# Optimization experiments

Hardware: AMD Instinct MI355X
Metric: run time of the kernel (lower is better)

## Reference

```python
import jax, jax.numpy as jnp
import numpy as np

B, L, S, D = 16, 32, 128, 256
WIN = 9
NEG = -1e10
EPS = 1e-6


def _band_mask(seq_len, win_size):
    half = win_size // 2
    i = jnp.arange(seq_len)
    m = jnp.abs(i[:, None] - i[None, :]) <= half
    return m[None, None, :, :]


def setup_inputs() -> dict:
    key = jax.random.key(0)
    ks = jax.random.split(key, 12)
    H_s = jax.random.normal(ks[0], (B, L, S, D), dtype=jnp.float32)
    seg_mask = jnp.ones((B, L, 1, S), dtype=bool)
    s = 0.02
    return {
        "H_s": H_s,
        "seg_mask": seg_mask,
        "Wq": jax.random.normal(ks[1], (D, D), jnp.float32) * s,
        "Wk": jax.random.normal(ks[2], (D, D), jnp.float32) * s,
        "Wv": jax.random.normal(ks[3], (D, D), jnp.float32) * s,
        "Wh_w": jax.random.normal(ks[4], (D, 1), jnp.float32) * s,
        "Wh_b": jnp.zeros((1,), jnp.float32),
        "Wg_w": jax.random.normal(ks[5], (D, 1), jnp.float32) * s,
        "Wl_w": jax.random.normal(ks[6], (D, 1), jnp.float32) * s,
        "ln_g": jnp.ones((D,), jnp.float32),
        "ln_b": jnp.zeros((D,), jnp.float32),
        "feat_simi": _band_mask(S, WIN),
    }


def reference(H_s, seg_mask, Wq, Wk, Wv, Wh_w, Wh_b, Wg_w, Wl_w, ln_g, ln_b, feat_simi):
    d = H_s.shape[-1]
    scaling = jnp.asarray(d, H_s.dtype) ** 0.5
    Q = H_s @ Wq
    K = H_s @ Wk
    V = H_s @ Wv
    # shared scores, computed once: (B, L, S, S)
    GP = jnp.einsum('blqd,blkd->blqk', Q / scaling, K)
    GP = jnp.where(seg_mask, GP, NEG)  # global path mask
    G_Att = jnp.einsum('blqk,blkd->blqd', jax.nn.softmax(GP, axis=-1), V)
    LP = jnp.where(feat_simi, GP, NEG)  # local window mask on top
    L_Att = jnp.einsum('blqk,blkd->blqd', jax.nn.softmax(LP, axis=-1), V)
    gate = jax.nn.sigmoid((H_s @ Wh_w + Wh_b) + G_Att @ Wg_w + L_Att @ Wl_w)
    Fusion = gate * L_Att + (1.0 - gate) * G_Att
    x = Fusion + H_s
    mu = jnp.mean(x, axis=-1, keepdims=True)
    var = jnp.var(x, axis=-1, keepdims=True)
    return ln_g * (x - mu) / jnp.sqrt(var + EPS) + ln_b
```

## Files before the change

kernel.cpp:

```cpp
#include <hip/hip_runtime.h>
#include <hip/hip_bf16.h>
#include <stdint.h>


#define NBL   512
#define SS    128
#define DD    256
#define BLKT  512
#define QSTR  264
#define VSTR  136
#define WSTR  40
#define NEGF  (-1e10f)

#define OFF_Q    0
#define OFF_KV   (SS * QSTR * 2)
#define KV_BYTES (DD * VSTR * 2)
#define OFF_W5   (OFF_KV + KV_BYTES)
#define SMEM_BYTES (OFF_W5 + 5 * DD * 4)
#define BUF_BYTES (DD * WSTR * 2)

typedef __attribute__((ext_vector_type(8))) short bf16x8;
typedef __attribute__((ext_vector_type(4))) float floatx4;

__device__ __forceinline__ uint32_t f2bf1(float f) {
  uint32_t u = __float_as_uint(f);
  return (u + 0x7fffu + ((u >> 16) & 1u)) >> 16;
}
__device__ __forceinline__ short f2bs(float f) { return (short)f2bf1(f); }
__device__ __forceinline__ uint32_t packbf(float a, float b) {
  return f2bf1(a) | (f2bf1(b) << 16);
}
__device__ __forceinline__ float qredSum(float v) {
  v += __shfl_xor(v, 1, 64); v += __shfl_xor(v, 2, 64);
  v += __shfl_xor(v, 4, 64); v += __shfl_xor(v, 8, 64);
  return v;
}
__device__ __forceinline__ float qredMax(float v) {
  v = fmaxf(v, __shfl_xor(v, 1, 64)); v = fmaxf(v, __shfl_xor(v, 2, 64));
  v = fmaxf(v, __shfl_xor(v, 4, 64)); v = fmaxf(v, __shfl_xor(v, 8, 64));
  return v;
}

#define LBAR() asm volatile("s_waitcnt lgkmcnt(0)\n\ts_barrier" ::: "memory")

#define LD_SLICE(DST, KS)                                          \
  {                                                                \
    _Pragma("unroll")                                              \
    for (int i = 0; i < 4; ++i) {                                  \
      const int ge = (KS) * 32 + (eb0 + 2 * i) * 4;                \
      _Pragma("unroll")                                            \
      for (int j = 0; j < 4; ++j)                                  \
        (DST)[i * 4 + j] = W[(ge + j) * DD + gd];                  \
    }                                                              \
  }

#define ST_SLICE(BUF, SRC)                                         \
  {                                                                \
    _Pragma("unroll")                                              \
    for (int i = 0; i < 4; ++i) {                                  \
      const int e = (eb0 + 2 * i) * 4;                             \
      *(uint2*)((BUF) + gd * WSTR + e) =                           \
          make_uint2(packbf((SRC)[i * 4 + 0], (SRC)[i * 4 + 1]),   \
                     packbf((SRC)[i * 4 + 2], (SRC)[i * 4 + 3]));  \
    }                                                              \
  }

#define PITER(KS, CURW, NXTW, CURBUF)                              \
  {                                                                \
    if ((KS) < 7) LD_SLICE(NXTW, (KS) + 1);                        \
    ST_SLICE(CURBUF, CURW);                                        \
    LBAR();                                                        \
    _Pragma("unroll")                                              \
    for (int nt = 0; nt < 16; ++nt) {                              \
      const bf16x8 b = *(const bf16x8*)((CURBUF) + (nt * 16 + n) * WSTR + quad * 8); \
      acc[nt] = __builtin_amdgcn_mfma_f32_16x16x32_bf16(a[KS], b, acc[nt], 0, 0, 0); \
    }                                                              \
  }

template <int TR, bool GUARD>
__device__ __forceinline__ void proj_pipe(const bf16x8* __restrict__ a,
                                          const float* __restrict__ W,
                                          uint16_t* __restrict__ dst, int dstStride,
                                          uint16_t* __restrict__ buf0,
                                          uint16_t* __restrict__ buf1,
                                          int tid, int m0, int n, int quad) {
  floatx4 acc[16];
#pragma unroll
  for (int i = 0; i < 16; ++i) acc[i] = (floatx4){0.f, 0.f, 0.f, 0.f};
  const int gd  = tid & 255;
  const int eb0 = tid >> 8;
  float wA[16], wB[16];

  LD_SLICE(wA, 0);
  PITER(0, wA, wB, buf0)  PITER(1, wB, wA, buf1)
  PITER(2, wA, wB, buf0)  PITER(3, wB, wA, buf1)
  PITER(4, wA, wB, buf0)  PITER(5, wB, wA, buf1)
  PITER(6, wA, wB, buf0)  PITER(7, wB, wA, buf1)

  if (GUARD) LBAR();

#pragma unroll
  for (int nt = 0; nt < 16; ++nt) {
    if (TR == 0) {
#pragma unroll
      for (int r = 0; r < 4; ++r)
        dst[(m0 + quad * 4 + r) * dstStride + nt * 16 + n] = (uint16_t)f2bf1(acc[nt][r]);
    } else {
      *(uint2*)(dst + (nt * 16 + n) * dstStride + m0 + quad * 4) =
          make_uint2(packbf(acc[nt][0], acc[nt][1]), packbf(acc[nt][2], acc[nt][3]));
    }
  }
  if (GUARD) LBAR();
}

__global__ __launch_bounds__(BLKT, 2) void segatt_kernel(
    const float* __restrict__ Hs, const float* __restrict__ Wq,
    const float* __restrict__ Wk, const float* __restrict__ Wv,
    const float* __restrict__ Whw, const float* __restrict__ Whb,
    const float* __restrict__ Wgw, const float* __restrict__ Wlw,
    const float* __restrict__ lng, const float* __restrict__ lnb,
    float* __restrict__ Out) {
  extern __shared__ __align__(16) char smem[];
  uint16_t* sQ   = (uint16_t*)(smem + OFF_Q);
  uint16_t* sK   = (uint16_t*)(smem + OFF_KV);
  uint16_t* sVT  = (uint16_t*)(smem + OFF_KV);
  uint16_t* buf0 = (uint16_t*)(smem + OFF_KV);
  uint16_t* buf1 = (uint16_t*)(smem + OFF_KV + BUF_BYTES);
  float*    sW5  = (float*)(smem + OFF_W5);

  const int tid  = threadIdx.x;
  const int bl   = blockIdx.x;
  const int lane = tid & 63;
  const int n    = lane & 15;
  const int quad = lane >> 4;
  const int m0   = (tid >> 6) * 16;
  const float* Hbl = Hs + (size_t)bl * SS * DD;
  float*       Obl = Out + (size_t)bl * SS * DD;
  const float Whb0 = Whb[0];

  for (int i = tid; i < 5 * DD; i += BLKT) {
    const int j = i & (DD - 1);
    const int m = i >> 8;
    sW5[i] = (m == 0) ? Whw[j] : (m == 1) ? Wgw[j] : (m == 2) ? Wlw[j]
           : (m == 3) ? lng[j] : lnb[j];
  }

  bf16x8 a[8];
#pragma unroll
  for (int ks = 0; ks < 8; ++ks) {
    const float* hp = Hbl + (m0 + n) * DD + ks * 32 + quad * 8;
    const float4 h0 = *(const float4*)hp;
    const float4 h1 = *(const float4*)(hp + 4);
    a[ks][0] = f2bs(h0.x); a[ks][1] = f2bs(h0.y); a[ks][2] = f2bs(h0.z); a[ks][3] = f2bs(h0.w);
    a[ks][4] = f2bs(h1.x); a[ks][5] = f2bs(h1.y); a[ks][6] = f2bs(h1.z); a[ks][7] = f2bs(h1.w);
  }

  proj_pipe<0, false>(a, Wq, sQ, QSTR, buf0, buf1, tid, m0, n, quad);
  proj_pipe<0, true >(a, Wk, sK, QSTR, buf0, buf1, tid, m0, n, quad);

  {
    floatx4 gp[8];
#pragma unroll
    for (int i = 0; i < 8; ++i) gp[i] = (floatx4){0.f, 0.f, 0.f, 0.f};
    for (int ks = 0; ks < 8; ++ks) {
      const bf16x8 aq = *(const bf16x8*)(sQ + (m0 + n) * QSTR + ks * 32 + quad * 8);
#pragma unroll
      for (int nt = 0; nt < 8; ++nt) {
        const bf16x8 bk = *(const bf16x8*)(sK + (nt * 16 + n) * QSTR + ks * 32 + quad * 8);
        gp[nt] = __builtin_amdgcn_mfma_f32_16x16x32_bf16(aq, bk, gp[nt], 0, 0, 0);
      }
    }
#pragma unroll
    for (int r = 0; r < 4; ++r) {
      const int q = m0 + quad * 4 + r;
      float g[8], e[8];
      float vm = -3.0e38f;
#pragma unroll
      for (int nt = 0; nt < 8; ++nt) { g[nt] = gp[nt][r] * 0.0625f; vm = fmaxf(vm, g[nt]); }
      const float rm = qredMax(vm);
      float s = 0.f;
#pragma unroll
      for (int nt = 0; nt < 8; ++nt) { e[nt] = __expf(g[nt] - rm); s += e[nt]; }
      const float inv = 1.f / qredSum(s);
      uint16_t* row = sQ + q * QSTR;
#pragma unroll
      for (int nt = 0; nt < 8; ++nt) row[nt * 16 + n] = (uint16_t)f2bf1(e[nt] * inv);
      float lvm = -3.0e38f;
#pragma unroll
      for (int nt = 0; nt < 8; ++nt) {
        const int kk = nt * 16 + n;
        int dk = q - kk; if (dk < 0) dk = -dk;
        g[nt] = (dk <= 4) ? g[nt] : NEGF;
        lvm = fmaxf(lvm, g[nt]);
      }
      const float lm = qredMax(lvm);
      float ls = 0.f;
#pragma unroll
      for (int nt = 0; nt < 8; ++nt) { e[nt] = __expf(g[nt] - lm); ls += e[nt]; }
      const float linv = 1.f / qredSum(ls);
#pragma unroll
      for (int nt = 0; nt < 8; ++nt) row[128 + nt * 16 + n] = (uint16_t)f2bf1(e[nt] * linv);
    }
  }
  LBAR();

  proj_pipe<1, true>(a, Wv, sVT, VSTR, buf0, buf1, tid, m0, n, quad);

  {
    floatx4 ag[16], al[16];
#pragma unroll
    for (int i = 0; i < 16; ++i) {
      ag[i] = (floatx4){0.f, 0.f, 0.f, 0.f};
      al[i] = (floatx4){0.f, 0.f, 0.f, 0.f};
    }
    for (int ks = 0; ks < 4; ++ks) {
      const bf16x8 ap = *(const bf16x8*)(sQ + (m0 + n) * QSTR + ks * 32 + quad * 8);
#pragma unroll
      for (int nt = 0; nt < 16; ++nt) {
        const bf16x8 bv = *(const bf16x8*)(sVT + (nt * 16 + n) * VSTR + ks * 32 + quad * 8);
        ag[nt] = __builtin_amdgcn_mfma_f32_16x16x32_bf16(ap, bv, ag[nt], 0, 0, 0);
      }
    }
    int sLo = m0 - 4;  if (sLo < 0) sLo = 0;
    int sHi = m0 + 19; if (sHi > SS - 1) sHi = SS - 1;
    for (int ks = sLo >> 5; ks <= (sHi >> 5); ++ks) {
      const bf16x8 ap = *(const bf16x8*)(sQ + (m0 + n) * QSTR + 128 + ks * 32 + quad * 8);
#pragma unroll
      for (int nt = 0; nt < 16; ++nt) {
        const bf16x8 bv = *(const bf16x8*)(sVT + (nt * 16 + n) * VSTR + ks * 32 + quad * 8);
        al[nt] = __builtin_amdgcn_mfma_f32_16x16x32_bf16(ap, bv, al[nt], 0, 0, 0);
      }
    }
#pragma unroll
    for (int r = 0; r < 4; ++r) {
      const int q = m0 + quad * 4 + r;
      const float* Hrow = Hbl + q * DD + n;
      float hv[16];
      float part = 0.f;
#pragma unroll
      for (int nt = 0; nt < 16; ++nt) {
        hv[nt] = Hrow[nt * 16];
        const int d = nt * 16 + n;
        part += hv[nt] * sW5[d] + ag[nt][r] * sW5[256 + d] + al[nt][r] * sW5[512 + d];
      }
      const float tot  = qredSum(part) + Whb0;
      const float gate = 1.f / (1.f + __expf(-tot));
      float s = 0.f, ss = 0.f;
#pragma unroll
      for (int nt = 0; nt < 16; ++nt) {
        const float x = gate * al[nt][r] + (1.f - gate) * ag[nt][r] + hv[nt];
        s += x; ss += x * x;
      }
      s = qredSum(s); ss = qredSum(ss);
      const float mu   = s * (1.f / 256.f);
      const float var  = ss * (1.f / 256.f) - mu * mu;
      const float rstd = rsqrtf(var + 1e-6f);
      float* Orow = Obl + q * DD + n;
#pragma unroll
      for (int nt = 0; nt < 16; ++nt) {
        const int d = nt * 16 + n;
        const float x = gate * al[nt][r] + (1.f - gate) * ag[nt][r] + hv[nt];
        Orow[nt * 16] = sW5[768 + d] * (x - mu) * rstd + sW5[1024 + d];
      }
    }
  }
}

extern "C" void kernel_launch(void* const* d_in, const int* in_sizes, int n_in,
                              void* d_out, int out_size, void* d_ws, size_t ws_size,
                              hipStream_t stream) {
  const float* Hs  = (const float*)d_in[0];
  const float* Wq  = (const float*)d_in[2];
  const float* Wk  = (const float*)d_in[3];
  const float* Wv  = (const float*)d_in[4];
  const float* Whw = (const float*)d_in[5];
  const float* Whb = (const float*)d_in[6];
  const float* Wgw = (const float*)d_in[7];
  const float* Wlw = (const float*)d_in[8];
  const float* lng = (const float*)d_in[9];
  const float* lnb = (const float*)d_in[10];
  float* Out = (float*)d_out;

  (void)hipFuncSetAttribute((const void*)segatt_kernel,
                            hipFuncAttributeMaxDynamicSharedMemorySize, SMEM_BYTES);
  segatt_kernel<<<dim3(NBL), dim3(BLKT), SMEM_BYTES, stream>>>(
      Hs, Wq, Wk, Wv, Whw, Whb, Wgw, Wlw, lng, lnb, Out);
}
```

Before: 238.5 us.

## Double threads per block, splitting output columns across wave pairs

Raises the block from 512 to 1024 threads. Each pair of waves now shares a 16-row tile and splits the N dimension in half, which halves the per-thread accumulator registers in the projections, QK^T, PV and epilogue. Row reductions for the softmax max and sum, the gate dot product and the LayerNorm statistics are combined across the two halves through a new shared-memory scratch area with extra barriers. The aim is more waves in flight to hide latency, at the cost of extra synchronization, redundant H reloads from global memory, and launch bounds that now demand tighter register limits.

```diff
diff --git a/kernel.cpp b/kernel.cpp
--- a/kernel.cpp
+++ b/kernel.cpp
@@ -6,7 +6,7 @@
 #define NBL   512
 #define SS    128
 #define DD    256
-#define BLKT  512
+#define BLKT  1024
 #define QSTR  264
 #define VSTR  136
 #define WSTR  40
@@ -16,7 +16,8 @@
 #define OFF_KV   (SS * QSTR * 2)
 #define KV_BYTES (DD * VSTR * 2)
 #define OFF_W5   (OFF_KV + KV_BYTES)
-#define SMEM_BYTES (OFF_W5 + 5 * DD * 4)
+#define OFF_RED  (OFF_W5 + 5 * DD * 4)
+#define SMEM_BYTES (OFF_RED + 7 * 2 * SS * 4)
 #define BUF_BYTES (DD * WSTR * 2)
 
 typedef __attribute__((ext_vector_type(8))) short bf16x8;
@@ -46,23 +47,16 @@
 #define LD_SLICE(DST, KS)                                          \
   {                                                                \
     _Pragma("unroll")                                              \
-    for (int i = 0; i < 4; ++i) {                                  \
-      const int ge = (KS) * 32 + (eb0 + 2 * i) * 4;                \
-      _Pragma("unroll")                                            \
-      for (int j = 0; j < 4; ++j)                                  \
-        (DST)[i * 4 + j] = W[(ge + j) * DD + gd];                  \
-    }                                                              \
+    for (int j = 0; j < 8; ++j)                                    \
+      (DST)[j] = W[((KS) * 32 + kb * 8 + j) * DD + sd];            \
   }
 
 #define ST_SLICE(BUF, SRC)                                         \
   {                                                                \
-    _Pragma("unroll")                                              \
-    for (int i = 0; i < 4; ++i) {                                  \
-      const int e = (eb0 + 2 * i) * 4;                             \
-      *(uint2*)((BUF) + gd * WSTR + e) =                           \
-          make_uint2(packbf((SRC)[i * 4 + 0], (SRC)[i * 4 + 1]),   \
-                     packbf((SRC)[i * 4 + 2], (SRC)[i * 4 + 3]));  \
-    }                                                              \
+    *(uint2*)((BUF) + sd * WSTR + kb * 8) =                        \
+        make_uint2(packbf((SRC)[0], (SRC)[1]), packbf((SRC)[2], (SRC)[3])); \
+    *(uint2*)((BUF) + sd * WSTR + kb * 8 + 4) =                    \
+        make_uint2(packbf((SRC)[4], (SRC)[5]), packbf((SRC)[6], (SRC)[7])); \
   }
 
 #define PITER(KS, CURW, NXTW, CURBUF)                              \
@@ -71,9 +65,9 @@
     ST_SLICE(CURBUF, CURW);                                        \
     LBAR();                                                        \
     _Pragma("unroll")                                              \
-    for (int nt = 0; nt < 16; ++nt) {                              \
-      const bf16x8 b = *(const bf16x8*)((CURBUF) + (nt * 16 + n) * WSTR + quad * 8); \
-      acc[nt] = __builtin_amdgcn_mfma_f32_16x16x32_bf16(a[KS], b, acc[nt], 0, 0, 0); \
+    for (int nti = 0; nti < 8; ++nti) {                            \
+      const bf16x8 b = *(const bf16x8*)((CURBUF) + ((nt0 + nti) * 16 + n) * WSTR + quad * 8); \
+      acc[nti] = __builtin_amdgcn_mfma_f32_16x16x32_bf16(a[KS], b, acc[nti], 0, 0, 0); \
     }                                                              \
   }
 
@@ -83,13 +77,12 @@
                                           uint16_t* __restrict__ dst, int dstStride,
                                           uint16_t* __restrict__ buf0,
                                           uint16_t* __restrict__ buf1,
-                                          int tid, int m0, int n, int quad) {
-  floatx4 acc[16];
-#pragma unroll
-  for (int i = 0; i < 16; ++i) acc[i] = (floatx4){0.f, 0.f, 0.f, 0.f};
-  const int gd  = tid & 255;
-  const int eb0 = tid >> 8;
-  float wA[16], wB[16];
+                                          int sd, int kb, int nt0,
+                                          int m0, int n, int quad) {
+  floatx4 acc[8];
+#pragma unroll
+  for (int i = 0; i < 8; ++i) acc[i] = (floatx4){0.f, 0.f, 0.f, 0.f};
+  float wA[8], wB[8];
 
   LD_SLICE(wA, 0);
   PITER(0, wA, wB, buf0)  PITER(1, wB, wA, buf1)
@@ -100,20 +93,21 @@
   if (GUARD) LBAR();
 
 #pragma unroll
-  for (int nt = 0; nt < 16; ++nt) {
+  for (int nti = 0; nti < 8; ++nti) {
+    const int nt = nt0 + nti;
     if (TR == 0) {
 #pragma unroll
       for (int r = 0; r < 4; ++r)
-        dst[(m0 + quad * 4 + r) * dstStride + nt * 16 + n] = (uint16_t)f2bf1(acc[nt][r]);
+        dst[(m0 + quad * 4 + r) * dstStride + nt * 16 + n] = (uint16_t)f2bf1(acc[nti][r]);
     } else {
       *(uint2*)(dst + (nt * 16 + n) * dstStride + m0 + quad * 4) =
-          make_uint2(packbf(acc[nt][0], acc[nt][1]), packbf(acc[nt][2], acc[nt][3]));
+          make_uint2(packbf(acc[nti][0], acc[nti][1]), packbf(acc[nti][2], acc[nti][3]));
     }
   }
   if (GUARD) LBAR();
 }
 
-__global__ __launch_bounds__(BLKT, 2) void segatt_kernel(
+__global__ __launch_bounds__(BLKT, 4) void segatt_kernel(
     const float* __restrict__ Hs, const float* __restrict__ Wq,
     const float* __restrict__ Wk, const float* __restrict__ Wv,
     const float* __restrict__ Whw, const float* __restrict__ Whb,
@@ -127,13 +121,27 @@
   uint16_t* buf0 = (uint16_t*)(smem + OFF_KV);
   uint16_t* buf1 = (uint16_t*)(smem + OFF_KV + BUF_BYTES);
   float*    sW5  = (float*)(smem + OFF_W5);
+  float*    sRed = (float*)(smem + OFF_RED);
+  float*    sGM  = sRed;
+  float*    sLM  = sRed + 256;
+  float*    sGS  = sRed + 512;
+  float*    sLS  = sRed + 768;
+  float*    sE   = sRed + 1024;
+  float*    sF   = sRed + 1280;
+  float*    sGG  = sRed + 1536;
 
   const int tid  = threadIdx.x;
   const int bl   = blockIdx.x;
   const int lane = tid & 63;
   const int n    = lane & 15;
   const int quad = lane >> 4;
-  const int m0   = (tid >> 6) * 16;
+  const int wid  = tid >> 6;
+  const int h    = wid & 1;
+  const int m0   = (wid >> 1) * 16;
+  const int nt0  = h * 8;
+  const int h4   = h * 4;
+  const int sd   = tid & 255;
+  const int kb   = (tid >> 8) & 3;
   const float* Hbl = Hs + (size_t)bl * SS * DD;
   float*       Obl = Out + (size_t)bl * SS * DD;
   const float Whb0 = Whb[0];
@@ -155,70 +163,84 @@
     a[ks][4] = f2bs(h1.x); a[ks][5] = f2bs(h1.y); a[ks][6] = f2bs(h1.z); a[ks][7] = f2bs(h1.w);
   }
 
-  proj_pipe<0, false>(a, Wq, sQ, QSTR, buf0, buf1, tid, m0, n, quad);
-  proj_pipe<0, true >(a, Wk, sK, QSTR, buf0, buf1, tid, m0, n, quad);
+  proj_pipe<0, false>(a, Wq, sQ, QSTR, buf0, buf1, sd, kb, nt0, m0, n, quad);
+  proj_pipe<0, true >(a, Wk, sK, QSTR, buf0, buf1, sd, kb, nt0, m0, n, quad);
 
   {
-    floatx4 gp[8];
-#pragma unroll
-    for (int i = 0; i < 8; ++i) gp[i] = (floatx4){0.f, 0.f, 0.f, 0.f};
+    floatx4 gp[4];
+#pragma unroll
+    for (int i = 0; i < 4; ++i) gp[i] = (floatx4){0.f, 0.f, 0.f, 0.f};
     for (int ks = 0; ks < 8; ++ks) {
       const bf16x8 aq = *(const bf16x8*)(sQ + (m0 + n) * QSTR + ks * 32 + quad * 8);
 #pragma unroll
-      for (int nt = 0; nt < 8; ++nt) {
-        const bf16x8 bk = *(const bf16x8*)(sK + (nt * 16 + n) * QSTR + ks * 32 + quad * 8);
-        gp[nt] = __builtin_amdgcn_mfma_f32_16x16x32_bf16(aq, bk, gp[nt], 0, 0, 0);
-      }
-    }
-#pragma unroll
-    for (int r = 0; r < 4; ++r) {
-      const int q = m0 + quad * 4 + r;
-      float g[8], e[8];
-      float vm = -3.0e38f;
-#pragma unroll
-      for (int nt = 0; nt < 8; ++nt) { g[nt] = gp[nt][r] * 0.0625f; vm = fmaxf(vm, g[nt]); }
-      const float rm = qredMax(vm);
-      float s = 0.f;
-#pragma unroll
-      for (int nt = 0; nt < 8; ++nt) { e[nt] = __expf(g[nt] - rm); s += e[nt]; }
-      const float inv = 1.f / qredSum(s);
+      for (int nti = 0; nti < 4; ++nti) {
+        const bf16x8 bk = *(const bf16x8*)(sK + ((h4 + nti) * 16 + n) * QSTR + ks * 32 + quad * 8);
+        gp[nti] = __builtin_amdgcn_mfma_f32_16x16x32_bf16(aq, bk, gp[nti], 0, 0, 0);
+      }
+    }
+    float e[4][4], el[4][4];
+#pragma unroll
+    for (int r = 0; r < 4; ++r) {
+      const int q = m0 + quad * 4 + r;
+      float pm = -3.0e38f, plm = -3.0e38f;
+#pragma unroll
+      for (int nti = 0; nti < 4; ++nti) {
+        const float g = gp[nti][r] * 0.0625f;
+        e[r][nti] = g; pm = fmaxf(pm, g);
+        const int kk = (h4 + nti) * 16 + n;
+        int dk = q - kk; if (dk < 0) dk = -dk;
+        const float gl = (dk <= 4) ? g : NEGF;
+        el[r][nti] = gl; plm = fmaxf(plm, gl);
+      }
+      pm = qredMax(pm); plm = qredMax(plm);
+      if ((lane & 15) == 0) { sGM[q * 2 + h] = pm; sLM[q * 2 + h] = plm; }
+    }
+    LBAR();
+#pragma unroll
+    for (int r = 0; r < 4; ++r) {
+      const int q = m0 + quad * 4 + r;
+      const float rm = fmaxf(sGM[q * 2], sGM[q * 2 + 1]);
+      const float lm = fmaxf(sLM[q * 2], sLM[q * 2 + 1]);
+      float ps = 0.f, pls = 0.f;
+#pragma unroll
+      for (int nti = 0; nti < 4; ++nti) {
+        e[r][nti]  = __expf(e[r][nti]  - rm); ps  += e[r][nti];
+        el[r][nti] = __expf(el[r][nti] - lm); pls += el[r][nti];
+      }
+      ps = qredSum(ps); pls = qredSum(pls);
+      if ((lane & 15) == 0) { sGS[q * 2 + h] = ps; sLS[q * 2 + h] = pls; }
+    }
+    LBAR();
+#pragma unroll
+    for (int r = 0; r < 4; ++r) {
+      const int q = m0 + quad * 4 + r;
+      const float inv  = 1.f / (sGS[q * 2] + sGS[q * 2 + 1]);
+      const float linv = 1.f / (sLS[q * 2] + sLS[q * 2 + 1]);
       uint16_t* row = sQ + q * QSTR;
 #pragma unroll
-      for (int nt = 0; nt < 8; ++nt) row[nt * 16 + n] = (uint16_t)f2bf1(e[nt] * inv);
-      float lvm = -3.0e38f;
-#pragma unroll
-      for (int nt = 0; nt < 8; ++nt) {
-        const int kk = nt * 16 + n;
-        int dk = q - kk; if (dk < 0) dk = -dk;
-        g[nt] = (dk <= 4) ? g[nt] : NEGF;
-        lvm = fmaxf(lvm, g[nt]);
-      }
-      const float lm = qredMax(lvm);
-      float ls = 0.f;
-#pragma unroll
-      for (int nt = 0; nt < 8; ++nt) { e[nt] = __expf(g[nt] - lm); ls += e[nt]; }
-      const float linv = 1.f / qredSum(ls);
-#pragma unroll
-      for (int nt = 0; nt < 8; ++nt) row[128 + nt * 16 + n] = (uint16_t)f2bf1(e[nt] * linv);
-    }
-  }
-  LBAR();
-
-  proj_pipe<1, true>(a, Wv, sVT, VSTR, buf0, buf1, tid, m0, n, quad);
+      for (int nti = 0; nti < 4; ++nti) {
+        const int kk = (h4 + nti) * 16 + n;
+        row[kk]       = (uint16_t)f2bf1(e[r][nti]  * inv);
+        row[128 + kk] = (uint16_t)f2bf1(el[r][nti] * linv);
+      }
+    }
+  }
+
+  proj_pipe<1, true>(a, Wv, sVT, VSTR, buf0, buf1, sd, kb, nt0, m0, n, quad);
 
   {
-    floatx4 ag[16], al[16];
-#pragma unroll
-    for (int i = 0; i < 16; ++i) {
+    floatx4 ag[8], al[8];
+#pragma unroll
+    for (int i = 0; i < 8; ++i) {
       ag[i] = (floatx4){0.f, 0.f, 0.f, 0.f};
       al[i] = (floatx4){0.f, 0.f, 0.f, 0.f};
     }
     for (int ks = 0; ks < 4; ++ks) {
       const bf16x8 ap = *(const bf16x8*)(sQ + (m0 + n) * QSTR + ks * 32 + quad * 8);
 #pragma unroll
-      for (int nt = 0; nt < 16; ++nt) {
-        const bf16x8 bv = *(const bf16x8*)(sVT + (nt * 16 + n) * VSTR + ks * 32 + quad * 8);
-        ag[nt] = __builtin_amdgcn_mfma_f32_16x16x32_bf16(ap, bv, ag[nt], 0, 0, 0);
+      for (int nti = 0; nti < 8; ++nti) {
+        const bf16x8 bv = *(const bf16x8*)(sVT + ((nt0 + nti) * 16 + n) * VSTR + ks * 32 + quad * 8);
+        ag[nti] = __builtin_amdgcn_mfma_f32_16x16x32_bf16(ap, bv, ag[nti], 0, 0, 0);
       }
     }
     int sLo = m0 - 4;  if (sLo < 0) sLo = 0;
@@ -226,41 +248,61 @@
     for (int ks = sLo >> 5; ks <= (sHi >> 5); ++ks) {
       const bf16x8 ap = *(const bf16x8*)(sQ + (m0 + n) * QSTR + 128 + ks * 32 + quad * 8);
 #pragma unroll
-      for (int nt = 0; nt < 16; ++nt) {
-        const bf16x8 bv = *(const bf16x8*)(sVT + (nt * 16 + n) * VSTR + ks * 32 + quad * 8);
-        al[nt] = __builtin_amdgcn_mfma_f32_16x16x32_bf16(ap, bv, al[nt], 0, 0, 0);
-      }
-    }
-#pragma unroll
-    for (int r = 0; r < 4; ++r) {
-      const int q = m0 + quad * 4 + r;
-      const float* Hrow = Hbl + q * DD + n;
-      float hv[16];
+      for (int nti = 0; nti < 8; ++nti) {
+        const bf16x8 bv = *(const bf16x8*)(sVT + ((nt0 + nti) * 16 + n) * VSTR + ks * 32 + quad * 8);
+        al[nti] = __builtin_amdgcn_mfma_f32_16x16x32_bf16(ap, bv, al[nti], 0, 0, 0);
+      }
+    }
+
+    const float* Hbase = Hbl + h * 128 + n;
+#pragma unroll
+    for (int r = 0; r < 4; ++r) {
+      const int q = m0 + quad * 4 + r;
+      const float* Hrow = Hbase + q * DD;
       float part = 0.f;
 #pragma unroll
-      for (int nt = 0; nt < 16; ++nt) {
-        hv[nt] = Hrow[nt * 16];
-        const int d = nt * 16 + n;
-        part += hv[nt] * sW5[d] + ag[nt][r] * sW5[256 + d] + al[nt][r] * sW5[512 + d];
-      }
-      const float tot  = qredSum(part) + Whb0;
+      for (int nti = 0; nti < 8; ++nti) {
+        const float hv = Hrow[nti * 16];
+        const int d = h * 128 + nti * 16 + n;
+        part += hv * sW5[d] + ag[nti][r] * sW5[256 + d] + al[nti][r] * sW5[512 + d];
+      }
+      part = qredSum(part);
+      if ((lane & 15) == 0) sE[q * 2 + h] = part;
+    }
+    LBAR();
+#pragma unroll
+    for (int r = 0; r < 4; ++r) {
+      const int q = m0 + quad * 4 + r;
+      const float* Hrow = Hbase + q * DD;
+      const float tot  = sE[q * 2] + sE[q * 2 + 1] + Whb0;
       const float gate = 1.f / (1.f + __expf(-tot));
       float s = 0.f, ss = 0.f;
 #pragma unroll
-      for (int nt = 0; nt < 16; ++nt) {
-        const float x = gate * al[nt][r] + (1.f - gate) * ag[nt][r] + hv[nt];
+      for (int nti = 0; nti < 8; ++nti) {
+        const float hv = Hrow[nti * 16];
+        const float x = gate * al[nti][r] + (1.f - gate) * ag[nti][r] + hv;
         s += x; ss += x * x;
       }
       s = qredSum(s); ss = qredSum(ss);
-      const float mu   = s * (1.f / 256.f);
-      const float var  = ss * (1.f / 256.f) - mu * mu;
+      if ((lane & 15) == 0) { sF[q * 2 + h] = s; sGG[q * 2 + h] = ss; }
+    }
+    LBAR();
+#pragma unroll
+    for (int r = 0; r < 4; ++r) {
+      const int q = m0 + quad * 4 + r;
+      const float* Hrow = Hbase + q * DD;
+      const float tot  = sE[q * 2] + sE[q * 2 + 1] + Whb0;
+      const float gate = 1.f / (1.f + __expf(-tot));
+      const float mu   = (sF[q * 2] + sF[q * 2 + 1]) * (1.f / 256.f);
+      const float var  = (sGG[q * 2] + sGG[q * 2 + 1]) * (1.f / 256.f) - mu * mu;
       const float rstd = rsqrtf(var + 1e-6f);
-      float* Orow = Obl + q * DD + n;
-#pragma unroll
-      for (int nt = 0; nt < 16; ++nt) {
-        const int d = nt * 16 + n;
-        const float x = gate * al[nt][r] + (1.f - gate) * ag[nt][r] + hv[nt];
-        Orow[nt * 16] = sW5[768 + d] * (x - mu) * rstd + sW5[1024 + d];
+      float* Orow = Obl + q * DD + h * 128 + n;
+#pragma unroll
+      for (int nti = 0; nti < 8; ++nti) {
+        const float hv = Hrow[nti * 16];
+        const int d = h * 128 + nti * 16 + n;
+        const float x = gate * al[nti][r] + (1.f - gate) * ag[nti][r] + hv;
+        Orow[nti * 16] = sW5[768 + d] * (x - mu) * rstd + sW5[1024 + d];
       }
     }
   }
```

Result: slower. 244.2 us (+2.4%).
